# Kernel optimization log

Hardware: AMD Instinct MI355X
Metric: run time of the kernel (lower is better)

Reference implementation:

```python
import jax, jax.numpy as jnp
import numpy as np

H = 32  # hidden size

def _lstm_layer(x, Wih, Whh, bih, bhh):
    # x: [B, T, in]; Wih: [4H, in]; Whh: [4H, H]; biases: [4H]
    # Precompute input contribution for all timesteps (one big GEMM).
    xg = jnp.einsum('bti,gi->btg', x, Wih) + (bih + bhh)  # [B, T, 4H]
    B = x.shape[0]
    h0 = jnp.zeros((B, H), x.dtype)
    c0 = jnp.zeros((B, H), x.dtype)

    def step(carry, xt):
        h, c = carry
        g = xt + h @ Whh.T                      # [B, 4H]
        i, f, gg, o = jnp.split(g, 4, axis=-1)   # PyTorch gate order: i,f,g,o
        i = jax.nn.sigmoid(i)
        f = jax.nn.sigmoid(f)
        gg = jnp.tanh(gg)
        o = jax.nn.sigmoid(o)
        c = f * c + i * gg
        h = o * jnp.tanh(c)
        return (h, c), h

    (_, _), hs = jax.lax.scan(step, (h0, c0), jnp.swapaxes(xg, 0, 1))  # hs: [T, B, H]
    return jnp.swapaxes(hs, 0, 1)  # [B, T, H]


def setup_inputs() -> dict:
    key = jax.random.key(0)
    ks = jax.random.split(key, 11)
    B, T = 4096, 1024
    s = 1.0 / np.sqrt(H)  # PyTorch LSTM init scale
    f32 = jnp.float32
    return {
        'x':    jax.random.normal(ks[0], (B, T, 1), dtype=f32),
        'Wih0': jax.random.uniform(ks[1], (4 * H, 1), dtype=f32, minval=-s, maxval=s),
        'Whh0': jax.random.uniform(ks[2], (4 * H, H), dtype=f32, minval=-s, maxval=s),
        'bih0': jax.random.uniform(ks[3], (4 * H,), dtype=f32, minval=-s, maxval=s),
        'bhh0': jax.random.uniform(ks[4], (4 * H,), dtype=f32, minval=-s, maxval=s),
        'Wih1': jax.random.uniform(ks[5], (4 * H, H), dtype=f32, minval=-s, maxval=s),
        'Whh1': jax.random.uniform(ks[6], (4 * H, H), dtype=f32, minval=-s, maxval=s),
        'bih1': jax.random.uniform(ks[7], (4 * H,), dtype=f32, minval=-s, maxval=s),
        'bhh1': jax.random.uniform(ks[8], (4 * H,), dtype=f32, minval=-s, maxval=s),
        'Wfc':  jax.random.uniform(ks[9], (1, H), dtype=f32, minval=-s, maxval=s),
        'bfc':  jax.random.uniform(ks[10], (1,), dtype=f32, minval=-s, maxval=s),
    }


def reference(x, Wih0, Whh0, bih0, bhh0, Wih1, Whh1, bih1, bhh1, Wfc, bfc):
    h1 = _lstm_layer(x, Wih0, Whh0, bih0, bhh0)   # [B, T, H]
    h2 = _lstm_layer(h1, Wih1, Whh1, bih1, bhh1)  # [B, T, H]
    last = h2[:, -1, :]                            # [B, H]
    return last @ Wfc.T + bfc                      # [B, 1]
```

## Files before the change

### kernel.cpp

```cpp
#include <hip/hip_runtime.h>

#define HSZ  32
#define TLEN 1024
#define PS   40

typedef _Float16 half8 __attribute__((ext_vector_type(8)));
typedef float    f32x4 __attribute__((ext_vector_type(4)));

__device__ __forceinline__ float rcp_f(float x){ return __builtin_amdgcn_rcpf(x); }
__device__ __forceinline__ float exp2_f(float x){ return __builtin_amdgcn_exp2f(x); }
#define LOG2E 1.442695040888963f
__device__ __forceinline__ float sigmoid_f(float x){ return rcp_f(1.0f + exp2_f(-LOG2E*x)); }
__device__ __forceinline__ float tanh_fast(float x){ return 1.0f - 2.0f*rcp_f(1.0f + exp2_f(2.0f*LOG2E*x)); }
__device__ __forceinline__ f32x4 mfma16(half8 a, half8 b, f32x4 c){
  return __builtin_amdgcn_mfma_f32_16x16x32_f16(a, b, c, 0, 0, 0);
}

__device__ __forceinline__ void lds_barrier(){
  asm volatile("s_waitcnt lgkmcnt(0)\n\ts_barrier" ::: "memory");
}

__global__ __launch_bounds__(512, 2) void lstm2_mfma8(
    const float* __restrict__ x,
    const float* __restrict__ Wih0, const float* __restrict__ Whh0,
    const float* __restrict__ bih0, const float* __restrict__ bhh0,
    const float* __restrict__ Wih1, const float* __restrict__ Whh1,
    const float* __restrict__ bih1, const float* __restrict__ bhh1,
    const float* __restrict__ Wfc,  const float* __restrict__ bfc,
    float* __restrict__ out, int Tn)
{
  __shared__ __align__(16) _Float16 hpl[2][2][16*PS];

  const int tid = threadIdx.x;
  const int w   = tid >> 6;
  const int l   = tid & 63;
  const int col = l & 15;
  const int g   = l >> 4;
  const int s   = 4*w + g;
  const int b0  = blockIdx.x * 16;

  const int prow = 32*(col & 3) + 4*w + (col >> 2);
  half8 W0h, W0l, WIh, WIl, WHh, WHl;
  {
    const float* p0 = Whh0 + prow*HSZ + 8*g;
    const float* p1 = Wih1 + prow*HSZ + 8*g;
    const float* p2 = Whh1 + prow*HSZ + 8*g;
    #pragma unroll
    for (int j = 0; j < 8; ++j){
      float v0 = p0[j], v1 = p1[j], v2 = p2[j];
      _Float16 a = (_Float16)v0; W0h[j] = a; W0l[j] = (_Float16)(v0 - (float)a);
      _Float16 b = (_Float16)v1; WIh[j] = b; WIl[j] = (_Float16)(v1 - (float)b);
      _Float16 c = (_Float16)v2; WHh[j] = c; WHl[j] = (_Float16)(v2 - (float)c);
    }
  }
  float wx[4], bs0[4];
  f32x4 bias1;
  #pragma unroll
  for (int j = 0; j < 4; ++j){
    int r    = 32*j + s;
    wx[j]    = Wih0[r];
    bs0[j]   = bih0[r] + bhh0[r];
    bias1[j] = bih1[r] + bhh1[r];
  }
  const f32x4 zero4 = {0.f, 0.f, 0.f, 0.f};

  const int wrI = col*PS + s;
  const int rdI = col*PS + 8*g;

  for (int i = tid; i < 2*2*16*PS; i += 512) (&hpl[0][0][0])[i] = (_Float16)0.0f;

  const float* xp = x + (size_t)(b0 + col) * Tn;
  float c0, c1 = 0.f, h1v = 0.f;

  {
    float x0 = xp[0];
    float e0 = fmaf(x0, wx[0], bs0[0]);
    float e2 = fmaf(x0, wx[2], bs0[2]);
    float e3 = fmaf(x0, wx[3], bs0[3]);
    float i0 = sigmoid_f(e0);
    float g0 = tanh_fast(e2);
    float o0 = sigmoid_f(e3);
    c0 = i0 * g0;
    float h0 = o0 * tanh_fast(c0);
    __syncthreads();
    hpl[0][0][wrI] = (_Float16)h0;
  }
  __syncthreads();
  half8 Bh0 = *(const half8*)&hpl[0][0][rdI];
  half8 Bh1 = *(const half8*)&hpl[0][1][rdI];
  float xv = xp[1];

#define STEP(Q, TIDX)                                                      \
  {                                                                        \
    float xn = xp[(TIDX)];               \
    f32x4 e;                                                               \
    e[0] = fmaf(xv, wx[0], bs0[0]);                                        \
    e[1] = fmaf(xv, wx[1], bs0[1]);                                        \
    e[2] = fmaf(xv, wx[2], bs0[2]);                                        \
    e[3] = fmaf(xv, wx[3], bs0[3]);                                        \
    f32x4 u, vv;                                                           \
    __builtin_amdgcn_s_setprio(1);                                         \
    e  = mfma16(W0h, Bh0, e);                                              \
    u  = mfma16(WHh, Bh1, bias1);                                          \
    vv = mfma16(WIh, Bh0, zero4);                                          \
    e  = mfma16(W0l, Bh0, e);                                              \
    u  = mfma16(WHl, Bh1, u);                                              \
    vv = mfma16(WIl, Bh0, vv);                                             \
    __builtin_amdgcn_s_setprio(0);                                         \
                                                                \
    float i1 = sigmoid_f(u[0] + vv[0]), f1 = sigmoid_f(u[1] + vv[1]);      \
    float g1 = tanh_fast(u[2] + vv[2]), o1 = sigmoid_f(u[3] + vv[3]);      \
    c1 = fmaf(f1, c1, i1 * g1);                                            \
    h1v = o1 * tanh_fast(c1);                                              \
    hpl[(Q)][1][wrI] = (_Float16)h1v;                                      \
                                                              \
    float i0 = sigmoid_f(e[0]), f0 = sigmoid_f(e[1]);                      \
    float g0 = tanh_fast(e[2]), o0 = sigmoid_f(e[3]);                      \
    c0 = fmaf(f0, c0, i0 * g0);                                            \
    float h0 = o0 * tanh_fast(c0);                                         \
    hpl[(Q)][0][wrI] = (_Float16)h0;                                       \
    lds_barrier();                                                         \
    Bh0 = *(const half8*)&hpl[(Q)][0][rdI];                                \
    Bh1 = *(const half8*)&hpl[(Q)][1][rdI];                                \
    xv = xn;                                                               \
  }

  for (int T0 = 0; T0 < Tn; T0 += 4){
    STEP(1, T0 + 2);
    STEP(0, T0 + 3);
    STEP(1, (T0 + 4 < Tn) ? T0 + 4 : Tn - 1);
    STEP(0, (T0 + 5 < Tn) ? T0 + 5 : Tn - 1);
  }
#undef STEP

  __syncthreads();
  float* sc = (float*)&hpl[0][0][0];
  sc[s*17 + col] = h1v;
  __syncthreads();
  if (tid < 16){
    float acc = bfc[0];
    #pragma unroll 8
    for (int k = 0; k < HSZ; ++k) acc = fmaf(sc[k*17 + tid], Wfc[k], acc);
    out[b0 + tid] = acc;
  }
}

extern "C" void kernel_launch(void* const* d_in, const int* in_sizes, int n_in,
                              void* d_out, int out_size, void* d_ws, size_t ws_size,
                              hipStream_t stream) {
  const float* x    = (const float*)d_in[0];
  const float* Wih0 = (const float*)d_in[1];
  const float* Whh0 = (const float*)d_in[2];
  const float* bih0 = (const float*)d_in[3];
  const float* bhh0 = (const float*)d_in[4];
  const float* Wih1 = (const float*)d_in[5];
  const float* Whh1 = (const float*)d_in[6];
  const float* bih1 = (const float*)d_in[7];
  const float* bhh1 = (const float*)d_in[8];
  const float* Wfc  = (const float*)d_in[9];
  const float* bfc  = (const float*)d_in[10];
  float* out = (float*)d_out;

  const int Tn = TLEN;
  const int B  = in_sizes[0] / Tn;

  dim3 block(512);
  dim3 grid(B / 16);
  hipLaunchKernelGGL(lstm2_mfma8, grid, block, 0, stream,
                     x, Wih0, Whh0, bih0, bhh0, Wih1, Whh1, bih1, bhh1,
                     Wfc, bfc, out, Tn);
}
```

Before: 427.0 us.

## Fold activation scales into weights, share reciprocals, and split layer steps

Pre-scales the weights and biases by -log2e, or 2*log2e for the g gate, so the gate pre-activations feed exp2 directly with no extra multiply. Gate activations are paired so that one reciprocal covers two sigmoid/tanh evaluations. The double-buffered LDS ping-pong with one barrier per step is replaced by single buffers with two barriers per step, and the layer-1 and layer-0 updates are interleaved around those barriers. This cuts transcendental and multiply work on the serial recurrence, but adds a second barrier to each timestep.

```diff
diff --git a/kernel.cpp b/kernel.cpp
--- a/kernel.cpp
+++ b/kernel.cpp
@@ -9,18 +9,34 @@
 
 __device__ __forceinline__ float rcp_f(float x){ return __builtin_amdgcn_rcpf(x); }
 __device__ __forceinline__ float exp2_f(float x){ return __builtin_amdgcn_exp2f(x); }
-#define LOG2E 1.442695040888963f
-__device__ __forceinline__ float sigmoid_f(float x){ return rcp_f(1.0f + exp2_f(-LOG2E*x)); }
-__device__ __forceinline__ float tanh_fast(float x){ return 1.0f - 2.0f*rcp_f(1.0f + exp2_f(2.0f*LOG2E*x)); }
+#define SCL_S (-1.442695040888963f)
+#define SCL_T ( 2.885390081777927f)
+
 __device__ __forceinline__ f32x4 mfma16(half8 a, half8 b, f32x4 c){
   return __builtin_amdgcn_mfma_f32_16x16x32_f16(a, b, c, 0, 0, 0);
 }
-
 __device__ __forceinline__ void lds_barrier(){
   asm volatile("s_waitcnt lgkmcnt(0)\n\ts_barrier" ::: "memory");
 }
 
-__global__ __launch_bounds__(512, 2) void lstm2_mfma8(
+#define ACT4(A0,A1,A2,A3, CV, OV)                              \
+  float OV;                                                    \
+  { float Zi_ = exp2_f(A0), Zf_ = exp2_f(A1);                  \
+    float Zg_ = exp2_f(A2), Zo_ = exp2_f(A3);                  \
+    float di_ = 1.f+Zi_, df_ = 1.f+Zf_;                        \
+    float dg_ = 1.f+Zg_, dq_ = 1.f+Zo_;                        \
+    float r1_ = rcp_f(di_*df_);                                \
+    float IV_ = r1_*df_, FV_ = r1_*di_;                        \
+    float r2_ = rcp_f(dg_*dq_);                                \
+    float GV_ = fmaf(-2.f, r2_*dq_, 1.f); OV = r2_*dg_;        \
+    CV = fmaf(FV_, CV, IV_*GV_); }
+
+#define HOUT(CV, OV, HV)                                       \
+  { float Zc_ = exp2_f(SCL_T*(CV));                            \
+    float rc_ = rcp_f(1.f + Zc_);                              \
+    HV = fmaf(-2.f, rc_*(OV), OV); }
+
+__global__ __launch_bounds__(512, 2) void lstm2_sp(
     const float* __restrict__ x,
     const float* __restrict__ Wih0, const float* __restrict__ Whh0,
     const float* __restrict__ bih0, const float* __restrict__ bhh0,
@@ -29,17 +45,20 @@
     const float* __restrict__ Wfc,  const float* __restrict__ bfc,
     float* __restrict__ out, int Tn)
 {
-  __shared__ __align__(16) _Float16 hpl[2][2][16*PS];
+  __shared__ __align__(16) _Float16 H0[16*PS];
+  __shared__ __align__(16) _Float16 H1[16*PS];
+  __shared__ float sc[32*17];
 
   const int tid = threadIdx.x;
   const int w   = tid >> 6;
   const int l   = tid & 63;
-  const int col = l & 15;
+  const int c   = l & 15;
   const int g   = l >> 4;
   const int s   = 4*w + g;
   const int b0  = blockIdx.x * 16;
 
-  const int prow = 32*(col & 3) + 4*w + (col >> 2);
+  const int prow = 32*(c & 3) + 4*w + (c >> 2);
+  const float sA = ((c & 3) == 2) ? SCL_T : SCL_S;
   half8 W0h, W0l, WIh, WIl, WHh, WHl;
   {
     const float* p0 = Whh0 + prow*HSZ + 8*g;
@@ -47,95 +66,96 @@
     const float* p2 = Whh1 + prow*HSZ + 8*g;
     #pragma unroll
     for (int j = 0; j < 8; ++j){
-      float v0 = p0[j], v1 = p1[j], v2 = p2[j];
+      float v0 = p0[j]*sA, v1 = p1[j]*sA, v2 = p2[j]*sA;
       _Float16 a = (_Float16)v0; W0h[j] = a; W0l[j] = (_Float16)(v0 - (float)a);
       _Float16 b = (_Float16)v1; WIh[j] = b; WIl[j] = (_Float16)(v1 - (float)b);
-      _Float16 c = (_Float16)v2; WHh[j] = c; WHl[j] = (_Float16)(v2 - (float)c);
+      _Float16 d = (_Float16)v2; WHh[j] = d; WHl[j] = (_Float16)(v2 - (float)d);
     }
   }
+  const float scj[4] = {SCL_S, SCL_S, SCL_T, SCL_S};
   float wx[4], bs0[4];
   f32x4 bias1;
   #pragma unroll
   for (int j = 0; j < 4; ++j){
     int r    = 32*j + s;
-    wx[j]    = Wih0[r];
-    bs0[j]   = bih0[r] + bhh0[r];
-    bias1[j] = bih1[r] + bhh1[r];
+    wx[j]    = Wih0[r] * scj[j];
+    bs0[j]   = (bih0[r] + bhh0[r]) * scj[j];
+    bias1[j] = (bih1[r] + bhh1[r]) * scj[j];
   }
   const f32x4 zero4 = {0.f, 0.f, 0.f, 0.f};
 
-  const int wrI = col*PS + s;
-  const int rdI = col*PS + 8*g;
+  const int wrI = c*PS + s;
+  const int rdI = c*PS + 8*g;
 
-  for (int i = tid; i < 2*2*16*PS; i += 512) (&hpl[0][0][0])[i] = (_Float16)0.0f;
-
-  const float* xp = x + (size_t)(b0 + col) * Tn;
-  float c0, c1 = 0.f, h1v = 0.f;
+  const float* xp = x + (size_t)(b0 + c) * Tn;
+  float c0 = 0.f, c1 = 0.f;
 
   {
     float x0 = xp[0];
-    float e0 = fmaf(x0, wx[0], bs0[0]);
-    float e2 = fmaf(x0, wx[2], bs0[2]);
-    float e3 = fmaf(x0, wx[3], bs0[3]);
-    float i0 = sigmoid_f(e0);
-    float g0 = tanh_fast(e2);
-    float o0 = sigmoid_f(e3);
-    c0 = i0 * g0;
-    float h0 = o0 * tanh_fast(c0);
-    __syncthreads();
-    hpl[0][0][wrI] = (_Float16)h0;
+    float a0 = fmaf(x0, wx[0], bs0[0]);
+    float a1 = fmaf(x0, wx[1], bs0[1]);
+    float a2 = fmaf(x0, wx[2], bs0[2]);
+    float a3 = fmaf(x0, wx[3], bs0[3]);
+    ACT4(a0, a1, a2, a3, c0, o0_);
+    float h0;
+    HOUT(c0, o0_, h0);
+    H0[wrI] = (_Float16)h0;
   }
   __syncthreads();
-  half8 Bh0 = *(const half8*)&hpl[0][0][rdI];
-  half8 Bh1 = *(const half8*)&hpl[0][1][rdI];
+  half8 Bh0 = *(const half8*)&H0[rdI];
+  half8 Bh1 = {};
   float xv = xp[1];
 
-#define STEP(Q, TIDX)                                                      \
-  {                                                                        \
-    float xn = xp[(TIDX)];               \
-    f32x4 e;                                                               \
-    e[0] = fmaf(xv, wx[0], bs0[0]);                                        \
-    e[1] = fmaf(xv, wx[1], bs0[1]);                                        \
-    e[2] = fmaf(xv, wx[2], bs0[2]);                                        \
-    e[3] = fmaf(xv, wx[3], bs0[3]);                                        \
-    f32x4 u, vv;                                                           \
-    __builtin_amdgcn_s_setprio(1);                                         \
-    e  = mfma16(W0h, Bh0, e);                                              \
-    u  = mfma16(WHh, Bh1, bias1);                                          \
-    vv = mfma16(WIh, Bh0, zero4);                                          \
-    e  = mfma16(W0l, Bh0, e);                                              \
-    u  = mfma16(WHl, Bh1, u);                                              \
-    vv = mfma16(WIl, Bh0, vv);                                             \
-    __builtin_amdgcn_s_setprio(0);                                         \
-                                                                \
-    float i1 = sigmoid_f(u[0] + vv[0]), f1 = sigmoid_f(u[1] + vv[1]);      \
-    float g1 = tanh_fast(u[2] + vv[2]), o1 = sigmoid_f(u[3] + vv[3]);      \
-    c1 = fmaf(f1, c1, i1 * g1);                                            \
-    h1v = o1 * tanh_fast(c1);                                              \
-    hpl[(Q)][1][wrI] = (_Float16)h1v;                                      \
-                                                              \
-    float i0 = sigmoid_f(e[0]), f0 = sigmoid_f(e[1]);                      \
-    float g0 = tanh_fast(e[2]), o0 = sigmoid_f(e[3]);                      \
-    c0 = fmaf(f0, c0, i0 * g0);                                            \
-    float h0 = o0 * tanh_fast(c0);                                         \
-    hpl[(Q)][0][wrI] = (_Float16)h0;                                       \
-    lds_barrier();                                                         \
-    Bh0 = *(const half8*)&hpl[(Q)][0][rdI];                                \
-    Bh1 = *(const half8*)&hpl[(Q)][1][rdI];                                \
-    xv = xn;                                                               \
+  float h1v = 0.f;
+  const int Tm1 = Tn - 1;
+
+  for (int t = 0; t < Tm1; ++t){
+    int xi = t + 2; xi = (xi > Tm1) ? Tm1 : xi;
+    float xn = xp[xi];
+
+    f32x4 u, vv;
+    u  = mfma16(WHh, Bh1, bias1);
+    u  = mfma16(WHl, Bh1, u);
+    vv = mfma16(WIh, Bh0, zero4);
+    vv = mfma16(WIl, Bh0, vv);
+    f32x4 a = u + vv;
+    ACT4(a[0], a[1], a[2], a[3], c1, o1_);
+    HOUT(c1, o1_, h1v);
+    H1[wrI] = (_Float16)h1v;
+
+    lds_barrier();
+
+    f32x4 e;
+    e[0] = fmaf(xv, wx[0], bs0[0]);
+    e[1] = fmaf(xv, wx[1], bs0[1]);
+    e[2] = fmaf(xv, wx[2], bs0[2]);
+    e[3] = fmaf(xv, wx[3], bs0[3]);
+    e = mfma16(W0h, Bh0, e);
+    e = mfma16(W0l, Bh0, e);
+    Bh1 = *(const half8*)&H1[rdI];
+    ACT4(e[0], e[1], e[2], e[3], c0, o0_);
+    float h0;
+    HOUT(c0, o0_, h0);
+    H0[wrI] = (_Float16)h0;
+
+    lds_barrier();
+
+    Bh0 = *(const half8*)&H0[rdI];
+    xv = xn;
   }
 
-  for (int T0 = 0; T0 < Tn; T0 += 4){
-    STEP(1, T0 + 2);
-    STEP(0, T0 + 3);
-    STEP(1, (T0 + 4 < Tn) ? T0 + 4 : Tn - 1);
-    STEP(0, (T0 + 5 < Tn) ? T0 + 5 : Tn - 1);
+  {
+    f32x4 u, vv;
+    u  = mfma16(WHh, Bh1, bias1);
+    u  = mfma16(WHl, Bh1, u);
+    vv = mfma16(WIh, Bh0, zero4);
+    vv = mfma16(WIl, Bh0, vv);
+    f32x4 a = u + vv;
+    ACT4(a[0], a[1], a[2], a[3], c1, o1_);
+    HOUT(c1, o1_, h1v);
   }
-#undef STEP
 
-  __syncthreads();
-  float* sc = (float*)&hpl[0][0][0];
-  sc[s*17 + col] = h1v;
+  sc[s*17 + c] = h1v;
   __syncthreads();
   if (tid < 16){
     float acc = bfc[0];
@@ -166,7 +186,7 @@
 
   dim3 block(512);
   dim3 grid(B / 16);
-  hipLaunchKernelGGL(lstm2_mfma8, grid, block, 0, stream,
+  hipLaunchKernelGGL(lstm2_sp, grid, block, 0, stream,
                      x, Wih0, Whh0, bih0, bhh0, Wih1, Whh1, bih1, bhh1,
                      Wfc, bfc, out, Tn);
 }
```

Result: slower. 499.3 us (+16.9%).
